# Kernel tuning notes

Measured on AMD Instinct MI355X. Metric: run time of the kernel, lower is better.

## Reference

```python
import jax, jax.numpy as jnp
import numpy as np

D_MODEL = 512
N_HEADS = 8
D_K = D_MODEL // N_HEADS  # 64
EPS = 1e-5


def setup_inputs() -> dict:
    key = jax.random.key(0)
    ks = jax.random.split(key, 16)
    s = 0.02
    B, T = 4, 2048
    return {
        "x": jax.random.normal(ks[0], (B, T, D_MODEL), dtype=jnp.float32),
        # per-head q/k/v projections stacked over heads: [H, d_model, d_k]
        "Wq": jax.random.normal(ks[1], (N_HEADS, D_MODEL, D_K), dtype=jnp.float32) * s,
        "bq": jnp.zeros((N_HEADS, D_K), dtype=jnp.float32),
        "Wk": jax.random.normal(ks[2], (N_HEADS, D_MODEL, D_K), dtype=jnp.float32) * s,
        "bk": jnp.zeros((N_HEADS, D_K), dtype=jnp.float32),
        "Wv": jax.random.normal(ks[3], (N_HEADS, D_MODEL, D_K), dtype=jnp.float32) * s,
        "bv": jnp.zeros((N_HEADS, D_K), dtype=jnp.float32),
        "Wp": jax.random.normal(ks[4], (D_MODEL, D_MODEL), dtype=jnp.float32) * s,
        "bp": jnp.zeros((D_MODEL,), dtype=jnp.float32),
        "W1": jax.random.normal(ks[5], (D_MODEL, 4 * D_MODEL), dtype=jnp.float32) * s,
        "b1": jnp.zeros((4 * D_MODEL,), dtype=jnp.float32),
        "W2": jax.random.normal(ks[6], (4 * D_MODEL, D_MODEL), dtype=jnp.float32) * s,
        "b2": jnp.zeros((D_MODEL,), dtype=jnp.float32),
        "g1": jnp.ones((D_MODEL,), dtype=jnp.float32),
        "be1": jnp.zeros((D_MODEL,), dtype=jnp.float32),
        "g2": jnp.ones((D_MODEL,), dtype=jnp.float32),
        "be2": jnp.zeros((D_MODEL,), dtype=jnp.float32),
    }


def _layer_norm(x, g, b):
    mu = jnp.mean(x, axis=-1, keepdims=True)
    var = jnp.var(x, axis=-1, keepdims=True)
    return (x - mu) * jax.lax.rsqrt(var + EPS) * g + b


def _block(x, Wq, bq, Wk, bk, Wv, bv, Wp, bp, W1, b1, W2, b2, g1, be1, g2, be2):
    B, T, _ = x.shape
    h = _layer_norm(x, g1, be1)
    # batched per-head projections: [B, H, T, d_k]
    q = jnp.einsum('btd,hdk->bhtk', h, Wq) + bq[:, None, :]
    k = jnp.einsum('btd,hdk->bhtk', h, Wk) + bk[:, None, :]
    v = jnp.einsum('btd,hdk->bhtk', h, Wv) + bv[:, None, :]
    scores = jnp.einsum('bhtk,bhsk->bhts', q, k)  # [B, H, T, T]
    causal = jnp.tril(jnp.ones((T, T), dtype=bool))
    # faithful to source: mask with -1e9 BEFORE dividing by sqrt(d_k)
    scores = jnp.where(causal, scores, jnp.float32(-1e9))
    attn = jax.nn.softmax(scores / jnp.float32(np.sqrt(D_K)), axis=-1)
    o = jnp.einsum('bhts,bhsk->bhtk', attn, v)  # [B, H, T, d_k]
    o = o.transpose(0, 2, 1, 3).reshape(B, T, D_MODEL)  # concat heads
    x = x + o @ Wp + bp
    h2 = _layer_norm(x, g2, be2)
    ff = jax.nn.relu(h2 @ W1 + b1) @ W2 + b2
    return x + ff


def reference(x, Wq, bq, Wk, bk, Wv, bv, Wp, bp, W1, b1, W2, b2, g1, be1, g2, be2):
    return _block(x, Wq, bq, Wk, bk, Wv, bv, Wp, bp, W1, b1, W2, b2, g1, be1, g2, be2)
```

## Files before the change

### kernel.cpp

```cpp
#include <hip/hip_runtime.h>
#include <hip/hip_bf16.h>
#include <math.h>

#define BATCH 4
#define SEQ   2048
#define DM    512
#define NH    8
#define DK    64
#define FF    2048
#define BT    (BATCH * SEQ)

#define SCALE_Q 0.18033688011112042f

typedef short bf16x8 __attribute__((ext_vector_type(8)));
typedef float f32x4  __attribute__((ext_vector_type(4)));

static __device__ inline short f2bf(float f) {
  union { float f; unsigned u; } v; v.f = f;
  unsigned r = (v.u + 0x7fffu + ((v.u >> 16) & 1u)) >> 16;
  return (short)r;
}

static __device__ __forceinline__ void gload16(const short* g, short* l) {
  __builtin_amdgcn_global_load_lds(
      (const __attribute__((address_space(1))) void*)g,
      (__attribute__((address_space(3))) void*)l, 16, 0, 0);
}

static __device__ __forceinline__ void xcd_swizzle(int& bx, int& by) {
  int gx = gridDim.x;
  int nwg = gx * gridDim.y;
  int id = blockIdx.x + gx * blockIdx.y;
  int nid = (id & 7) * (nwg >> 3) + (id >> 3);
  bx = nid % gx;
  by = nid / gx;
}

__global__ __launch_bounds__(256) void ln_kernel(
    const float* __restrict__ x, const float* __restrict__ gamma,
    const float* __restrict__ beta, short* __restrict__ out) {
  int row = blockIdx.x;
  const float* xr = x + (size_t)row * DM;
  int t = threadIdx.x;
  float v0 = xr[t], v1 = xr[t + 256];
  float s = v0 + v1;
  float sq = v0 * v0 + v1 * v1;
  for (int off = 32; off; off >>= 1) {
    s  += __shfl_xor(s, off);
    sq += __shfl_xor(sq, off);
  }
  __shared__ float ssum[4], ssq[4];
  int wave = t >> 6, lane = t & 63;
  if (lane == 0) { ssum[wave] = s; ssq[wave] = sq; }
  __syncthreads();
  if (t == 0) {
    float S = ssum[0] + ssum[1] + ssum[2] + ssum[3];
    float Q = ssq[0] + ssq[1] + ssq[2] + ssq[3];
    float mu = S * (1.0f / DM);
    float var = Q * (1.0f / DM) - mu * mu;
    ssum[0] = mu;
    ssq[0] = rsqrtf(var + 1e-5f);
  }
  __syncthreads();
  float mu = ssum[0], rstd = ssq[0];
  short* orow = out + (size_t)row * DM;
  orow[t]       = f2bf((v0 - mu) * rstd * gamma[t]       + beta[t]);
  orow[t + 256] = f2bf((v1 - mu) * rstd * gamma[t + 256] + beta[t + 256]);
}

__global__ __launch_bounds__(256) void wconv_kernel(
    const float* Wq, const float* Wk, const float* Wv,
    const float* Wp, const float* W1, const float* W2,
    short* wqkv, short* wpt, short* w1t, short* w2t) {
  int id = blockIdx.x;
  const float* src; short* dst; int R, C, tx, ty;
  if (id < 192) {
    int z = id >> 3;
    int m = z >> 3, hh = z & 7;
    const float* s0 = (m == 0) ? Wq : (m == 1) ? Wk : Wv;
    src = s0 + (size_t)hh * 512 * 64;
    dst = wqkv + ((size_t)(m * 512 + hh * 64)) * 512;
    R = 512; C = 64; tx = 0; ty = id & 7;
  } else if (id < 256) {
    int w = id - 192; src = Wp; dst = wpt; R = 512; C = 512;
    tx = w & 7; ty = w >> 3;
  } else if (id < 512) {
    int w = id - 256; src = W1; dst = w1t; R = 512; C = 2048;
    tx = w & 31; ty = w >> 5;
  } else {
    int w = id - 512; src = W2; dst = w2t; R = 2048; C = 512;
    tx = w & 7; ty = w >> 3;
  }
  __shared__ float Ts[64][68];
  int t = threadIdx.x;
  int r = t >> 2, c0 = (t & 3) * 16;
  const float* sp = src + (size_t)(ty * 64 + r) * C + tx * 64 + c0;
#pragma unroll
  for (int i = 0; i < 16; i += 4) {
    float4 v = *(const float4*)(sp + i);
    Ts[c0 + i + 0][r] = v.x; Ts[c0 + i + 1][r] = v.y;
    Ts[c0 + i + 2][r] = v.z; Ts[c0 + i + 3][r] = v.w;
  }
  __syncthreads();
  short* dp = dst + (size_t)(tx * 64 + r) * R + ty * 64 + c0;
  short tmp[16];
#pragma unroll
  for (int i = 0; i < 16; ++i) tmp[i] = f2bf(Ts[r][c0 + i]);
  *(int4*)(dp)     = *(int4*)&tmp[0];
  *(int4*)(dp + 8) = *(int4*)&tmp[8];
}

template<int TM, int TN>
__device__ __forceinline__ void gemm_core(
    const short* __restrict__ A, const short* __restrict__ Bw,
    int m0, int n0, int K, short* smem, f32x4 (&acc)[TM / 32][TN / 32]) {
  constexpr int AF = TM / 32, BF = TN / 32;
  constexpr int AC = TM / 64, BC = TN / 64;
  constexpr int BUFS = (TM + TN) * 32;
  int t = threadIdx.x;
  int wave = t >> 6, lane = t & 63, quad = lane >> 4, l16 = lane & 15;
  int wr = wave >> 1, wc = wave & 1;

  size_t aoff[AC], boff[BC];
  int aldsoff[AC], bldsoff[BC];
#pragma unroll
  for (int c = 0; c < AC; ++c) {
    int p = c * 256 + t, row = p >> 2, lg = (p & 3) ^ ((row >> 1) & 3);
    aoff[c] = (size_t)(m0 + row) * K + lg * 8;
    aldsoff[c] = c * 2048 + wave * 512;
  }
#pragma unroll
  for (int c = 0; c < BC; ++c) {
    int p = c * 256 + t, row = p >> 2, lg = (p & 3) ^ ((row >> 1) & 3);
    boff[c] = (size_t)(n0 + row) * K + lg * 8;
    bldsoff[c] = TM * 32 + c * 2048 + wave * 512;
  }

#pragma unroll
  for (int c = 0; c < AC; ++c) gload16(A + aoff[c], smem + aldsoff[c]);
#pragma unroll
  for (int c = 0; c < BC; ++c) gload16(Bw + boff[c], smem + bldsoff[c]);

  int physo = (quad ^ ((l16 >> 1) & 3)) * 8;

  for (int k0 = 0; k0 < K; k0 += 32) {
    short* cbuf = smem + ((k0 >> 5) & 1) * BUFS;
    __syncthreads();
    if (k0 + 32 < K) {
      short* nbuf = smem + (((k0 >> 5) & 1) ^ 1) * BUFS;
#pragma unroll
      for (int c = 0; c < AC; ++c) gload16(A + aoff[c] + k0 + 32, nbuf + aldsoff[c]);
#pragma unroll
      for (int c = 0; c < BC; ++c) gload16(Bw + boff[c] + k0 + 32, nbuf + bldsoff[c]);
    }
    bf16x8 af[AF], bfr[BF];
#pragma unroll
    for (int i = 0; i < AF; ++i)
      af[i] = *(const bf16x8*)&cbuf[(wr * (TM / 2) + i * 16 + l16) * 32 + physo];
#pragma unroll
    for (int j = 0; j < BF; ++j)
      bfr[j] = *(const bf16x8*)&cbuf[TM * 32 + (wc * (TN / 2) + j * 16 + l16) * 32 + physo];
#pragma unroll
    for (int i = 0; i < AF; ++i)
#pragma unroll
      for (int j = 0; j < BF; ++j)
        acc[i][j] = __builtin_amdgcn_mfma_f32_16x16x32_bf16(bfr[j], af[i], acc[i][j], 0, 0, 0);
  }
}

__global__ __launch_bounds__(256) void mgemm64_kernel(
    const short* __restrict__ A, const short* __restrict__ Bw,
    const float* __restrict__ bias, const float* __restrict__ res,
    void* __restrict__ C, int N, int K, int dorelu, int bf16out) {
  __shared__ __align__(16) short smem[2 * 8192];
  f32x4 acc[2][2];
  f32x4 zf = {0.f, 0.f, 0.f, 0.f};
#pragma unroll
  for (int i = 0; i < 2; ++i)
#pragma unroll
    for (int j = 0; j < 2; ++j) acc[i][j] = zf;
  int bx, by;
  xcd_swizzle(bx, by);
  int m0 = by * 64, n0 = bx * 64;

  int t = threadIdx.x;
  int wave = t >> 6, lane = t & 63, quad = lane >> 4, l16 = lane & 15;
  int wr = wave >> 1, wc = wave & 1;

  int rA0 = t >> 3,        lg0 = (t & 7) ^ (rA0 & 7);
  int rA1 = 32 + (t >> 3), lg1 = (t & 7) ^ (rA1 & 7);
  size_t aoff0 = (size_t)(m0 + rA0) * K + lg0 * 8;
  size_t aoff1 = (size_t)(m0 + rA1) * K + lg1 * 8;
  size_t boff0 = (size_t)(n0 + rA0) * K + lg0 * 8;
  size_t boff1 = (size_t)(n0 + rA1) * K + lg1 * 8;
  int lo0 = wave * 512, lo1 = 2048 + wave * 512;

  gload16(A + aoff0, smem + lo0);
  gload16(A + aoff1, smem + lo1);
  gload16(Bw + boff0, smem + 4096 + lo0);
  gload16(Bw + boff1, smem + 4096 + lo1);

  int sw = l16 & 7;

  for (int k0 = 0; k0 < K; k0 += 64) {
    short* cbuf = smem + ((k0 >> 6) & 1) * 8192;
    __syncthreads();
    if (k0 + 64 < K) {
      short* nbuf = smem + (((k0 >> 6) & 1) ^ 1) * 8192;
      gload16(A + aoff0 + k0 + 64, nbuf + lo0);
      gload16(A + aoff1 + k0 + 64, nbuf + lo1);
      gload16(Bw + boff0 + k0 + 64, nbuf + 4096 + lo0);
      gload16(Bw + boff1 + k0 + 64, nbuf + 4096 + lo1);
    }
    bf16x8 af0[2], af1[2], bf0[2], bf1[2];
#pragma unroll
    for (int i = 0; i < 2; ++i) {
      int r = wr * 32 + i * 16 + l16;
      af0[i] = *(const bf16x8*)&cbuf[r * 64 + ((quad ^ sw) * 8)];
      af1[i] = *(const bf16x8*)&cbuf[r * 64 + (((4 + quad) ^ sw) * 8)];
    }
#pragma unroll
    for (int j = 0; j < 2; ++j) {
      int r = wc * 32 + j * 16 + l16;
      bf0[j] = *(const bf16x8*)&cbuf[4096 + r * 64 + ((quad ^ sw) * 8)];
      bf1[j] = *(const bf16x8*)&cbuf[4096 + r * 64 + (((4 + quad) ^ sw) * 8)];
    }
#pragma unroll
    for (int i = 0; i < 2; ++i)
#pragma unroll
      for (int j = 0; j < 2; ++j) {
        acc[i][j] = __builtin_amdgcn_mfma_f32_16x16x32_bf16(bf0[j], af0[i], acc[i][j], 0, 0, 0);
        acc[i][j] = __builtin_amdgcn_mfma_f32_16x16x32_bf16(bf1[j], af1[i], acc[i][j], 0, 0, 0);
      }
  }

#pragma unroll
  for (int i = 0; i < 2; ++i) {
    int m = m0 + wr * 32 + i * 16 + l16;
#pragma unroll
    for (int j = 0; j < 2; ++j) {
      int nb = n0 + wc * 32 + j * 16 + quad * 4;
      float4 bv = *(const float4*)&bias[nb];
      float v[4] = {acc[i][j][0] + bv.x, acc[i][j][1] + bv.y,
                    acc[i][j][2] + bv.z, acc[i][j][3] + bv.w};
      if (dorelu) {
#pragma unroll
        for (int r = 0; r < 4; ++r) v[r] = fmaxf(v[r], 0.0f);
      }
      size_t off = (size_t)m * N + nb;
      if (res) {
        float4 rv = *(const float4*)(res + off);
        v[0] += rv.x; v[1] += rv.y; v[2] += rv.z; v[3] += rv.w;
      }
      if (bf16out) {
        short tmp[4] = {f2bf(v[0]), f2bf(v[1]), f2bf(v[2]), f2bf(v[3])};
        *(int2*)((short*)C + off) = *(int2*)tmp;
      } else {
        float4 outv = {v[0], v[1], v[2], v[3]};
        *(float4*)((float*)C + off) = outv;
      }
    }
  }
}

__global__ __launch_bounds__(256) void qkv_kernel(
    const short* __restrict__ A, const short* __restrict__ Bw,
    const float* __restrict__ bq, const float* __restrict__ bk,
    const float* __restrict__ bv,
    short* __restrict__ q, short* __restrict__ k, short* __restrict__ vt) {
  __shared__ __align__(16) short smem[12288];
  f32x4 acc[4][2];
  f32x4 zf = {0.f, 0.f, 0.f, 0.f};
#pragma unroll
  for (int i = 0; i < 4; ++i)
#pragma unroll
    for (int j = 0; j < 2; ++j) acc[i][j] = zf;
  int bx, by;
  xcd_swizzle(bx, by);
  int m0 = by * 128, n0 = bx * 64;
  gemm_core<128, 64>(A, Bw, m0, n0, DM, smem, acc);

  int t = threadIdx.x;
  int wave = t >> 6, lane = t & 63, quad = lane >> 4, l16 = lane & 15;
  int wr = wave >> 1, wc = wave & 1;

  if (n0 < 1024) {
    short* out = (n0 < 512) ? q : k;
    const float* bias = (n0 < 512) ? bq + n0 : bk + (n0 - 512);
    float scale = (n0 < 512) ? SCALE_Q : 1.0f;
    int ncol0 = (n0 < 512) ? n0 : n0 - 512;
#pragma unroll
    for (int i = 0; i < 4; ++i) {
      int m = m0 + wr * 64 + i * 16 + l16;
#pragma unroll
      for (int j = 0; j < 2; ++j) {
        int nb = wc * 32 + j * 16 + quad * 4;
        float4 bvv = *(const float4*)&bias[nb];
        short tmp[4];
        tmp[0] = f2bf((acc[i][j][0] + bvv.x) * scale);
        tmp[1] = f2bf((acc[i][j][1] + bvv.y) * scale);
        tmp[2] = f2bf((acc[i][j][2] + bvv.z) * scale);
        tmp[3] = f2bf((acc[i][j][3] + bvv.w) * scale);
        *(int2*)(out + (size_t)m * DM + ncol0 + nb) = *(int2*)tmp;
      }
    }
  } else {
    const float* bias = bv + (n0 - 1024);
    __syncthreads();
    short* Ts = smem;
#pragma unroll
    for (int i = 0; i < 4; ++i) {
      int ml = wr * 64 + i * 16 + l16;
#pragma unroll
      for (int j = 0; j < 2; ++j) {
        int nb = wc * 32 + j * 16 + quad * 4;
        float4 bvv = *(const float4*)&bias[nb];
        Ts[(nb + 0) * 136 + ml] = f2bf(acc[i][j][0] + bvv.x);
        Ts[(nb + 1) * 136 + ml] = f2bf(acc[i][j][1] + bvv.y);
        Ts[(nb + 2) * 136 + ml] = f2bf(acc[i][j][2] + bvv.z);
        Ts[(nb + 3) * 136 + ml] = f2bf(acc[i][j][3] + bvv.w);
      }
    }
    __syncthreads();
    int nl = t >> 2, seg = (t & 3) * 32;
    int gn = (n0 - 1024) + nl;
    int hh = gn >> 6, dk = gn & 63;
    int bidx = m0 >> 11, s0 = (m0 & 2047) + seg;
    short* dst = vt + ((size_t)((bidx * NH + hh) * DK + dk)) * SEQ + s0;
    const short* srcT = &Ts[nl * 136 + seg];
#pragma unroll
    for (int i2 = 0; i2 < 32; i2 += 8)
      *(int4*)(dst + i2) = *(const int4*)(srcT + i2);
  }
}

template<bool DIAG>
static __device__ __forceinline__ void attn_tile(
    const short* __restrict__ KsC, const short* __restrict__ VsC,
    short* __restrict__ Psw, const bf16x8& qf0, const bf16x8& qf1,
    f32x4 (&o_acc)[4], float& l_part, int quad, int l16,
    int keyb0, int qrow) {
  f32x4 zf = {0.f, 0.f, 0.f, 0.f};
  int sw = l16 & 7;

#pragma unroll
  for (int nt = 0; nt < 4; ++nt) {
    int krow = nt * 16 + l16;
    bf16x8 ka0 = *(const bf16x8*)&KsC[krow * 64 + ((quad ^ sw) * 8)];
    bf16x8 ka1 = *(const bf16x8*)&KsC[krow * 64 + (((4 + quad) ^ sw) * 8)];
    f32x4 s = __builtin_amdgcn_mfma_f32_16x16x32_bf16(ka0, qf0, zf, 0, 0, 0);
    s = __builtin_amdgcn_mfma_f32_16x16x32_bf16(ka1, qf1, s, 0, 0, 0);
    int keyb = keyb0 + nt * 16 + quad * 4;
    float pr[4];
#pragma unroll
    for (int r = 0; r < 4; ++r) {
      float e = exp2f(s[r]);
      pr[r] = (DIAG && (keyb + r > qrow)) ? 0.0f : e;
      l_part += pr[r];
    }
    unsigned pk0 = __builtin_amdgcn_perm(
        __float_as_uint(pr[1]), __float_as_uint(pr[0]), 0x07060302u);
    unsigned pk1 = __builtin_amdgcn_perm(
        __float_as_uint(pr[3]), __float_as_uint(pr[2]), 0x07060302u);
    int2 w = {(int)pk0, (int)pk1};
    *(int2*)&Psw[l16 * 64 + (((nt * 2 + (quad >> 1)) ^ sw) << 3) +
                 ((quad & 1) * 4)] = w;
  }

  bf16x8 apf0 = *(const bf16x8*)&Psw[l16 * 64 + ((quad ^ sw) * 8)];
  bf16x8 apf1 = *(const bf16x8*)&Psw[l16 * 64 + (((4 + quad) ^ sw) * 8)];
  __builtin_amdgcn_s_setprio(1);
#pragma unroll
  for (int nt2 = 0; nt2 < 4; ++nt2) {
    int vrow = nt2 * 16 + l16;
    bf16x8 vf0 = *(const bf16x8*)&VsC[vrow * 64 + ((quad ^ sw) * 8)];
    bf16x8 vf1 = *(const bf16x8*)&VsC[vrow * 64 + (((4 + quad) ^ sw) * 8)];
    o_acc[nt2] = __builtin_amdgcn_mfma_f32_16x16x32_bf16(vf0, apf0, o_acc[nt2], 0, 0, 0);
    o_acc[nt2] = __builtin_amdgcn_mfma_f32_16x16x32_bf16(vf1, apf1, o_acc[nt2], 0, 0, 0);
  }
  __builtin_amdgcn_s_setprio(0);
}

__global__ __launch_bounds__(256) void fattn_kernel(
    const short* __restrict__ Q, const short* __restrict__ Kg,
    const short* __restrict__ Vt, short* __restrict__ O,
    float* __restrict__ pscr) {
  int id = blockIdx.x;
  int c = id & 7, j = id >> 3;
  int sub = j & 3, w = j >> 2;
  int g = c * 4 + sub;
  int h = g & 7, b = g >> 3;
  int qt, kt0, ktN, p = 0;
  bool split;
  if (w < 16)      { qt = 31 - w;        p = 0; kt0 = 0;  ktN = 16;     split = true;  }
  else if (w < 32) { qt = 31 - (w - 16); p = 1; kt0 = 16; ktN = qt + 1; split = true;  }
  else             { qt = 15 - (w - 32);        kt0 = 0;  ktN = qt + 1; split = false; }
  bool hasdiag = !(split && p == 0);
  int q0 = qt * 64;
  int t = threadIdx.x, wave = t >> 6, lane = t & 63, quad = lane >> 4, l16 = lane & 15;

  __shared__ __align__(16) short Ks[2][64 * 64];
  __shared__ __align__(16) short Vs[2][64 * 64];
  __shared__ __align__(16) short Ps[4][16 * 64];

  f32x4 zf = {0.f, 0.f, 0.f, 0.f};
  const short* qp = Q + ((size_t)(b * SEQ + q0 + wave * 16 + l16)) * DM + h * DK;
  bf16x8 qf0 = *(const bf16x8*)(qp + quad * 8);
  bf16x8 qf1 = *(const bf16x8*)(qp + 32 + quad * 8);

  f32x4 o_acc[4];
  float l_part = 0.0f;
#pragma unroll
  for (int i = 0; i < 4; ++i) o_acc[i] = zf;

  const short* kb = Kg + ((size_t)(b * SEQ)) * DM + h * DK;
  const short* vb = Vt + ((size_t)((b * NH + h) * DK)) * SEQ;

  int row0 = t >> 3,         lg0 = (t & 7) ^ (row0 & 7);
  int row1 = (256 + t) >> 3, lg1 = ((256 + t) & 7) ^ (row1 & 7);
  const short* kp0 = kb + (size_t)row0 * DM + lg0 * 8 + (size_t)kt0 * 64 * DM;
  const short* kp1 = kb + (size_t)row1 * DM + lg1 * 8 + (size_t)kt0 * 64 * DM;
  const short* vp0 = vb + (size_t)row0 * SEQ + lg0 * 8 + kt0 * 64;
  const short* vp1 = vb + (size_t)row1 * SEQ + lg1 * 8 + kt0 * 64;
  int lo0 = wave * 512, lo1 = 2048 + wave * 512;

#define STAGE_KV(B) do {                                     \
    gload16(kp0, &Ks[B][lo0]); gload16(kp1, &Ks[B][lo1]);    \
    gload16(vp0, &Vs[B][lo0]); gload16(vp1, &Vs[B][lo1]);    \
    kp0 += 64 * DM; kp1 += 64 * DM; vp0 += 64; vp1 += 64; } while (0)

  STAGE_KV(0);

  int qrow = q0 + wave * 16 + l16;
  short* Psw = &Ps[wave][0];

  int buf = 0;
  for (int kt = kt0; kt < ktN - 1; ++kt) {
    __syncthreads();
    STAGE_KV(buf ^ 1);
    attn_tile<false>(&Ks[buf][0], &Vs[buf][0], Psw, qf0, qf1,
                     o_acc, l_part, quad, l16, 0, qrow);
    buf ^= 1;
  }
  __syncthreads();
  if (hasdiag)
    attn_tile<true>(&Ks[buf][0], &Vs[buf][0], Psw, qf0, qf1,
                    o_acc, l_part, quad, l16, (ktN - 1) * 64, qrow);
  else
    attn_tile<false>(&Ks[buf][0], &Vs[buf][0], Psw, qf0, qf1,
                     o_acc, l_part, quad, l16, 0, qrow);

  float lf = l_part;
  lf += __shfl_xor(lf, 16);
  lf += __shfl_xor(lf, 32);

  if (!split) {
    float inv = 1.0f / lf;
    short* orow = O + ((size_t)(b * SEQ) + qrow) * DM + h * DK;
#pragma unroll
    for (int nt2 = 0; nt2 < 4; ++nt2) {
      short tmp[4];
#pragma unroll
      for (int r = 0; r < 4; ++r) tmp[r] = f2bf(o_acc[nt2][r] * inv);
      *(int2*)(orow + nt2 * 16 + quad * 4) = *(int2*)tmp;
    }
  } else {
    int pblk = g * 16 + (qt - 16);
    int srow = pblk * 64 + wave * 16 + l16;
    float* po = pscr + (size_t)p * (32768 * 64);
    float* pl = pscr + (size_t)2 * (32768 * 64) + (size_t)p * 32768;
#pragma unroll
    for (int nt2 = 0; nt2 < 4; ++nt2)
      *(f32x4*)&po[(size_t)srow * 64 + nt2 * 16 + quad * 4] = o_acc[nt2];
    if (lane < 16) pl[pblk * 64 + wave * 16 + lane] = lf;
  }
#undef STAGE_KV
}

__global__ __launch_bounds__(256) void cmb_kernel(
    const float* __restrict__ pscr, short* __restrict__ O) {
  int gid = blockIdx.x * 256 + threadIdx.x;
  int srow = gid >> 6, dk = gid & 63;
  const float* po0 = pscr;
  const float* po1 = pscr + (size_t)32768 * 64;
  const float* pl0 = pscr + (size_t)2 * 32768 * 64;
  const float* pl1 = pl0 + 32768;
  float v = po0[gid] + po1[gid];
  float l = pl0[srow] + pl1[srow];
  int g = srow >> 10, rem = srow & 1023;
  int qt = 16 + (rem >> 6), row = rem & 63;
  int b = g >> 3, h = g & 7;
  int qrow = qt * 64 + row;
  O[((size_t)(b * SEQ + qrow)) * DM + h * DK + dk] = f2bf(v / l);
}

extern "C" void kernel_launch(void* const* d_in, const int* in_sizes, int n_in,
                              void* d_out, int out_size, void* d_ws, size_t ws_size,
                              hipStream_t stream) {
  const float* x   = (const float*)d_in[0];
  const float* Wq  = (const float*)d_in[1];
  const float* bq  = (const float*)d_in[2];
  const float* Wk  = (const float*)d_in[3];
  const float* bk  = (const float*)d_in[4];
  const float* Wv  = (const float*)d_in[5];
  const float* bv  = (const float*)d_in[6];
  const float* Wp  = (const float*)d_in[7];
  const float* bp  = (const float*)d_in[8];
  const float* W1  = (const float*)d_in[9];
  const float* b1  = (const float*)d_in[10];
  const float* W2  = (const float*)d_in[11];
  const float* b2  = (const float*)d_in[12];
  const float* g1  = (const float*)d_in[13];
  const float* be1 = (const float*)d_in[14];
  const float* g2  = (const float*)d_in[15];
  const float* be2 = (const float*)d_in[16];
  float* out = (float*)d_out;

  char* wsb = (char*)d_ws;
  const size_t SB = (size_t)BT * DM * 2;
  short* h    = (short*)(wsb);
  short* q    = (short*)(wsb + SB);
  short* k    = (short*)(wsb + 2 * SB);
  short* vt   = (short*)(wsb + 3 * SB);
  short* o    = (short*)(wsb + 4 * SB);
  float* x2   = (float*)(wsb + 5 * SB);
  short* h2   = (short*)(wsb + 5 * SB + (size_t)BT * DM * 4);
  short* ff   = (short*)(wsb + 6 * SB + (size_t)BT * DM * 4);
  float* pscr = (float*)ff;
  short* wqkv = (short*)(wsb + 6 * SB + (size_t)BT * DM * 4 + (size_t)BT * FF * 2);
  short* wpt  = wqkv + 1536 * 512;
  short* w1t  = wpt + 512 * 512;
  short* w2t  = w1t + 2048 * 512;

  dim3 blk(256);

  wconv_kernel<<<dim3(768), blk, 0, stream>>>(Wq, Wk, Wv, Wp, W1, W2,
                                              wqkv, wpt, w1t, w2t);
  ln_kernel<<<BT, blk, 0, stream>>>(x, g1, be1, h);

  qkv_kernel<<<dim3(24, 64), blk, 0, stream>>>(h, wqkv, bq, bk, bv, q, k, vt);

  fattn_kernel<<<dim3(1536), blk, 0, stream>>>(q, k, vt, o, pscr);
  cmb_kernel<<<dim3(8192), blk, 0, stream>>>(pscr, o);

  mgemm64_kernel<<<dim3(8, 128), blk, 0, stream>>>(o, wpt, bp, x, x2, DM, DM, 0, 0);
  ln_kernel<<<BT, blk, 0, stream>>>(x2, g2, be2, h2);
  mgemm64_kernel<<<dim3(32, 128), blk, 0, stream>>>(h2, w1t, b1, nullptr, ff, FF, DM, 1, 1);
  mgemm64_kernel<<<dim3(8, 128), blk, 0, stream>>>(ff, w2t, b2, x2, out, DM, FF, 0, 0);
}
```

Baseline: 251.4 us.

## Process two 16-row query groups per wave in flash attention to reuse K/V fragments

```diff
diff --git a/kernel.cpp b/kernel.cpp
--- a/kernel.cpp
+++ b/kernel.cpp
@@ -335,11 +335,11 @@
 }
 
 template<bool DIAG>
-static __device__ __forceinline__ void attn_tile(
+static __device__ __forceinline__ void attn_tile2(
     const short* __restrict__ KsC, const short* __restrict__ VsC,
-    short* __restrict__ Psw, const bf16x8& qf0, const bf16x8& qf1,
-    f32x4 (&o_acc)[4], float& l_part, int quad, int l16,
-    int keyb0, int qrow) {
+    short* __restrict__ Psw, const bf16x8 (&qf)[2][2],
+    f32x4 (&o_acc)[2][4], float (&lp)[2], int quad, int l16,
+    int keyb0, int qrow0, int qrow1) {
   f32x4 zf = {0.f, 0.f, 0.f, 0.f};
   int sw = l16 & 7;
 
@@ -348,35 +348,52 @@
     int krow = nt * 16 + l16;
     bf16x8 ka0 = *(const bf16x8*)&KsC[krow * 64 + ((quad ^ sw) * 8)];
     bf16x8 ka1 = *(const bf16x8*)&KsC[krow * 64 + (((4 + quad) ^ sw) * 8)];
-    f32x4 s = __builtin_amdgcn_mfma_f32_16x16x32_bf16(ka0, qf0, zf, 0, 0, 0);
-    s = __builtin_amdgcn_mfma_f32_16x16x32_bf16(ka1, qf1, s, 0, 0, 0);
-    int keyb = keyb0 + nt * 16 + quad * 4;
-    float pr[4];
+    f32x4 s0 = __builtin_amdgcn_mfma_f32_16x16x32_bf16(ka0, qf[0][0], zf, 0, 0, 0);
+    s0 = __builtin_amdgcn_mfma_f32_16x16x32_bf16(ka1, qf[0][1], s0, 0, 0, 0);
+    f32x4 s1 = __builtin_amdgcn_mfma_f32_16x16x32_bf16(ka0, qf[1][0], zf, 0, 0, 0);
+    s1 = __builtin_amdgcn_mfma_f32_16x16x32_bf16(ka1, qf[1][1], s1, 0, 0, 0);
+    int keyq = keyb0 + nt * 16 + quad * 4;
+    float p0[4], p1[4];
 #pragma unroll
     for (int r = 0; r < 4; ++r) {
-      float e = exp2f(s[r]);
-      pr[r] = (DIAG && (keyb + r > qrow)) ? 0.0f : e;
-      l_part += pr[r];
-    }
-    unsigned pk0 = __builtin_amdgcn_perm(
-        __float_as_uint(pr[1]), __float_as_uint(pr[0]), 0x07060302u);
-    unsigned pk1 = __builtin_amdgcn_perm(
-        __float_as_uint(pr[3]), __float_as_uint(pr[2]), 0x07060302u);
-    int2 w = {(int)pk0, (int)pk1};
-    *(int2*)&Psw[l16 * 64 + (((nt * 2 + (quad >> 1)) ^ sw) << 3) +
-                 ((quad & 1) * 4)] = w;
-  }
-
-  bf16x8 apf0 = *(const bf16x8*)&Psw[l16 * 64 + ((quad ^ sw) * 8)];
-  bf16x8 apf1 = *(const bf16x8*)&Psw[l16 * 64 + (((4 + quad) ^ sw) * 8)];
+      float e = exp2f(s0[r]);
+      p0[r] = (DIAG && (keyq + r > qrow0)) ? 0.0f : e;
+    }
+    lp[0] += (p0[0] + p0[1]) + (p0[2] + p0[3]);
+#pragma unroll
+    for (int r = 0; r < 4; ++r) {
+      float e = exp2f(s1[r]);
+      p1[r] = (DIAG && (keyq + r > qrow1)) ? 0.0f : e;
+    }
+    lp[1] += (p1[0] + p1[1]) + (p1[2] + p1[3]);
+    unsigned a0 = __builtin_amdgcn_perm(
+        __float_as_uint(p0[1]), __float_as_uint(p0[0]), 0x07060302u);
+    unsigned a1 = __builtin_amdgcn_perm(
+        __float_as_uint(p0[3]), __float_as_uint(p0[2]), 0x07060302u);
+    int2 w0 = {(int)a0, (int)a1};
+    *(int2*)&Psw[l16 * 72 + nt * 16 + quad * 4] = w0;
+    unsigned b0 = __builtin_amdgcn_perm(
+        __float_as_uint(p1[1]), __float_as_uint(p1[0]), 0x07060302u);
+    unsigned b1 = __builtin_amdgcn_perm(
+        __float_as_uint(p1[3]), __float_as_uint(p1[2]), 0x07060302u);
+    int2 w1 = {(int)b0, (int)b1};
+    *(int2*)&Psw[(16 + l16) * 72 + nt * 16 + quad * 4] = w1;
+  }
+
+  bf16x8 ap00 = *(const bf16x8*)&Psw[l16 * 72 + quad * 8];
+  bf16x8 ap01 = *(const bf16x8*)&Psw[l16 * 72 + 32 + quad * 8];
+  bf16x8 ap10 = *(const bf16x8*)&Psw[(16 + l16) * 72 + quad * 8];
+  bf16x8 ap11 = *(const bf16x8*)&Psw[(16 + l16) * 72 + 32 + quad * 8];
   __builtin_amdgcn_s_setprio(1);
 #pragma unroll
   for (int nt2 = 0; nt2 < 4; ++nt2) {
-    int vrow = nt2 * 16 + l16;
-    bf16x8 vf0 = *(const bf16x8*)&VsC[vrow * 64 + ((quad ^ sw) * 8)];
-    bf16x8 vf1 = *(const bf16x8*)&VsC[vrow * 64 + (((4 + quad) ^ sw) * 8)];
-    o_acc[nt2] = __builtin_amdgcn_mfma_f32_16x16x32_bf16(vf0, apf0, o_acc[nt2], 0, 0, 0);
-    o_acc[nt2] = __builtin_amdgcn_mfma_f32_16x16x32_bf16(vf1, apf1, o_acc[nt2], 0, 0, 0);
+    int vrow = nt2 * 16 + l16, swv = vrow & 7;
+    bf16x8 vf0 = *(const bf16x8*)&VsC[vrow * 64 + ((quad ^ swv) * 8)];
+    bf16x8 vf1 = *(const bf16x8*)&VsC[vrow * 64 + (((4 + quad) ^ swv) * 8)];
+    o_acc[0][nt2] = __builtin_amdgcn_mfma_f32_16x16x32_bf16(vf0, ap00, o_acc[0][nt2], 0, 0, 0);
+    o_acc[0][nt2] = __builtin_amdgcn_mfma_f32_16x16x32_bf16(vf1, ap01, o_acc[0][nt2], 0, 0, 0);
+    o_acc[1][nt2] = __builtin_amdgcn_mfma_f32_16x16x32_bf16(vf0, ap10, o_acc[1][nt2], 0, 0, 0);
+    o_acc[1][nt2] = __builtin_amdgcn_mfma_f32_16x16x32_bf16(vf1, ap11, o_acc[1][nt2], 0, 0, 0);
   }
   __builtin_amdgcn_s_setprio(0);
 }
@@ -387,31 +404,39 @@
     float* __restrict__ pscr) {
   int id = blockIdx.x;
   int c = id & 7, j = id >> 3;
-  int sub = j & 3, w = j >> 2;
-  int g = c * 4 + sub;
+  int g = c * 4 + (j & 3);
+  int w = j >> 2;
   int h = g & 7, b = g >> 3;
-  int qt, kt0, ktN, p = 0;
+  int s, kt0, ktN, p = 0;
   bool split;
-  if (w < 16)      { qt = 31 - w;        p = 0; kt0 = 0;  ktN = 16;     split = true;  }
-  else if (w < 32) { qt = 31 - (w - 16); p = 1; kt0 = 16; ktN = qt + 1; split = true;  }
-  else             { qt = 15 - (w - 32);        kt0 = 0;  ktN = qt + 1; split = false; }
+  if (w < 8)       { s = 15 - w;        p = 0; kt0 = 0;     ktN = s + 1;     split = true;  }
+  else if (w < 16) { s = 15 - (w - 8);  p = 1; kt0 = s + 1; ktN = 2 * s + 2; split = true;  }
+  else             { s = 7 - (w - 16);         kt0 = 0;     ktN = 2 * s + 2; split = false; }
   bool hasdiag = !(split && p == 0);
-  int q0 = qt * 64;
+  int q0 = s * 128;
   int t = threadIdx.x, wave = t >> 6, lane = t & 63, quad = lane >> 4, l16 = lane & 15;
 
   __shared__ __align__(16) short Ks[2][64 * 64];
   __shared__ __align__(16) short Vs[2][64 * 64];
-  __shared__ __align__(16) short Ps[4][16 * 64];
+  __shared__ __align__(16) short Ps[4][32 * 72];
 
   f32x4 zf = {0.f, 0.f, 0.f, 0.f};
-  const short* qp = Q + ((size_t)(b * SEQ + q0 + wave * 16 + l16)) * DM + h * DK;
-  bf16x8 qf0 = *(const bf16x8*)(qp + quad * 8);
-  bf16x8 qf1 = *(const bf16x8*)(qp + 32 + quad * 8);
-
-  f32x4 o_acc[4];
-  float l_part = 0.0f;
-#pragma unroll
-  for (int i = 0; i < 4; ++i) o_acc[i] = zf;
+  int qrow0 = q0 + wave * 32 + l16;
+  int qrow1 = qrow0 + 16;
+  const short* qp0 = Q + ((size_t)(b * SEQ + qrow0)) * DM + h * DK;
+  const short* qp1 = Q + ((size_t)(b * SEQ + qrow1)) * DM + h * DK;
+  bf16x8 qf[2][2];
+  qf[0][0] = *(const bf16x8*)(qp0 + quad * 8);
+  qf[0][1] = *(const bf16x8*)(qp0 + 32 + quad * 8);
+  qf[1][0] = *(const bf16x8*)(qp1 + quad * 8);
+  qf[1][1] = *(const bf16x8*)(qp1 + 32 + quad * 8);
+
+  f32x4 o_acc[2][4];
+  float lp[2] = {0.0f, 0.0f};
+#pragma unroll
+  for (int gi = 0; gi < 2; ++gi)
+#pragma unroll
+    for (int i = 0; i < 4; ++i) o_acc[gi][i] = zf;
 
   const short* kb = Kg + ((size_t)(b * SEQ)) * DM + h * DK;
   const short* vb = Vt + ((size_t)((b * NH + h) * DK)) * SEQ;
@@ -431,48 +456,47 @@
 
   STAGE_KV(0);
 
-  int qrow = q0 + wave * 16 + l16;
   short* Psw = &Ps[wave][0];
-
   int buf = 0;
-  for (int kt = kt0; kt < ktN - 1; ++kt) {
+  for (int kt = kt0; kt < ktN; ++kt) {
     __syncthreads();
-    STAGE_KV(buf ^ 1);
-    attn_tile<false>(&Ks[buf][0], &Vs[buf][0], Psw, qf0, qf1,
-                     o_acc, l_part, quad, l16, 0, qrow);
+    if (kt + 1 < ktN) STAGE_KV(buf ^ 1);
+    if (hasdiag && kt >= ktN - 2)
+      attn_tile2<true>(&Ks[buf][0], &Vs[buf][0], Psw, qf,
+                       o_acc, lp, quad, l16, kt * 64, qrow0, qrow1);
+    else
+      attn_tile2<false>(&Ks[buf][0], &Vs[buf][0], Psw, qf,
+                        o_acc, lp, quad, l16, 0, qrow0, qrow1);
     buf ^= 1;
   }
-  __syncthreads();
-  if (hasdiag)
-    attn_tile<true>(&Ks[buf][0], &Vs[buf][0], Psw, qf0, qf1,
-                    o_acc, l_part, quad, l16, (ktN - 1) * 64, qrow);
-  else
-    attn_tile<false>(&Ks[buf][0], &Vs[buf][0], Psw, qf0, qf1,
-                     o_acc, l_part, quad, l16, 0, qrow);
-
-  float lf = l_part;
-  lf += __shfl_xor(lf, 16);
-  lf += __shfl_xor(lf, 32);
-
-  if (!split) {
-    float inv = 1.0f / lf;
-    short* orow = O + ((size_t)(b * SEQ) + qrow) * DM + h * DK;
-#pragma unroll
-    for (int nt2 = 0; nt2 < 4; ++nt2) {
-      short tmp[4];
-#pragma unroll
-      for (int r = 0; r < 4; ++r) tmp[r] = f2bf(o_acc[nt2][r] * inv);
-      *(int2*)(orow + nt2 * 16 + quad * 4) = *(int2*)tmp;
-    }
-  } else {
-    int pblk = g * 16 + (qt - 16);
-    int srow = pblk * 64 + wave * 16 + l16;
-    float* po = pscr + (size_t)p * (32768 * 64);
-    float* pl = pscr + (size_t)2 * (32768 * 64) + (size_t)p * 32768;
-#pragma unroll
-    for (int nt2 = 0; nt2 < 4; ++nt2)
-      *(f32x4*)&po[(size_t)srow * 64 + nt2 * 16 + quad * 4] = o_acc[nt2];
-    if (lane < 16) pl[pblk * 64 + wave * 16 + lane] = lf;
+
+#pragma unroll
+  for (int gi = 0; gi < 2; ++gi) {
+    float lf = lp[gi];
+    lf += __shfl_xor(lf, 16);
+    lf += __shfl_xor(lf, 32);
+    int qrow = (gi == 0) ? qrow0 : qrow1;
+    if (!split) {
+      float inv = 1.0f / lf;
+      short* orow = O + ((size_t)(b * SEQ) + qrow) * DM + h * DK;
+#pragma unroll
+      for (int nt2 = 0; nt2 < 4; ++nt2) {
+        short tmp[4];
+#pragma unroll
+        for (int r = 0; r < 4; ++r) tmp[r] = f2bf(o_acc[gi][nt2][r] * inv);
+        *(int2*)(orow + nt2 * 16 + quad * 4) = *(int2*)tmp;
+      }
+    } else {
+      int pblk = g * 8 + (s - 8);
+      int lrow = wave * 32 + gi * 16 + l16;
+      int srow = pblk * 128 + lrow;
+      float* po = pscr + (size_t)p * (32768 * 64);
+      float* pl = pscr + (size_t)2 * (32768 * 64) + (size_t)p * 32768;
+#pragma unroll
+      for (int nt2 = 0; nt2 < 4; ++nt2)
+        *(f32x4*)&po[(size_t)srow * 64 + nt2 * 16 + quad * 4] = o_acc[gi][nt2];
+      if (lane < 16) pl[pblk * 128 + wave * 32 + gi * 16 + lane] = lf;
+    }
   }
 #undef STAGE_KV
 }
@@ -487,10 +511,10 @@
   const float* pl1 = pl0 + 32768;
   float v = po0[gid] + po1[gid];
   float l = pl0[srow] + pl1[srow];
-  int g = srow >> 10, rem = srow & 1023;
-  int qt = 16 + (rem >> 6), row = rem & 63;
+  int pblk = srow >> 7, r128 = srow & 127;
+  int g = pblk >> 3, s = 8 + (pblk & 7);
   int b = g >> 3, h = g & 7;
-  int qrow = qt * 64 + row;
+  int qrow = s * 128 + r128;
   O[((size_t)(b * SEQ + qrow)) * DM + h * DK + dk] = f2bf(v / l);
 }
 
@@ -540,7 +564,7 @@
 
   qkv_kernel<<<dim3(24, 64), blk, 0, stream>>>(h, wqkv, bq, bk, bv, q, k, vt);
 
-  fattn_kernel<<<dim3(1536), blk, 0, stream>>>(q, k, vt, o, pscr);
+  fattn_kernel<<<dim3(768), blk, 0, stream>>>(q, k, vt, o, pscr);
   cmb_kernel<<<dim3(8192), blk, 0, stream>>>(pscr, o);
 
   mgemm64_kernel<<<dim3(8, 128), blk, 0, stream>>>(o, wpt, bp, x, x2, DM, DM, 0, 0);
```

After: 270.1 us. 7.4% more time.

## Replace double-buffered LDS direct loads with register prefetch and single LDS buffer

Applied to the files above, without the earlier changes.

```diff
diff --git a/kernel.cpp b/kernel.cpp
--- a/kernel.cpp
+++ b/kernel.cpp
@@ -381,7 +381,7 @@
   __builtin_amdgcn_s_setprio(0);
 }
 
-__global__ __launch_bounds__(256) void fattn_kernel(
+__global__ __launch_bounds__(256, 6) void fattn_kernel(
     const short* __restrict__ Q, const short* __restrict__ Kg,
     const short* __restrict__ Vt, short* __restrict__ O,
     float* __restrict__ pscr) {
@@ -399,8 +399,8 @@
   int q0 = qt * 64;
   int t = threadIdx.x, wave = t >> 6, lane = t & 63, quad = lane >> 4, l16 = lane & 15;
 
-  __shared__ __align__(16) short Ks[2][64 * 64];
-  __shared__ __align__(16) short Vs[2][64 * 64];
+  __shared__ __align__(16) short Ks[64 * 64];
+  __shared__ __align__(16) short Vs[64 * 64];
   __shared__ __align__(16) short Ps[4][16 * 64];
 
   f32x4 zf = {0.f, 0.f, 0.f, 0.f};
@@ -422,33 +422,38 @@
   const short* kp1 = kb + (size_t)row1 * DM + lg1 * 8 + (size_t)kt0 * 64 * DM;
   const short* vp0 = vb + (size_t)row0 * SEQ + lg0 * 8 + kt0 * 64;
   const short* vp1 = vb + (size_t)row1 * SEQ + lg1 * 8 + kt0 * 64;
-  int lo0 = wave * 512, lo1 = 2048 + wave * 512;
-
-#define STAGE_KV(B) do {                                     \
-    gload16(kp0, &Ks[B][lo0]); gload16(kp1, &Ks[B][lo1]);    \
-    gload16(vp0, &Vs[B][lo0]); gload16(vp1, &Vs[B][lo1]);    \
+
+  int4 rk0, rk1, rv0, rv1;
+#define LOAD_KV() do {                                        \
+    rk0 = *(const int4*)kp0; rk1 = *(const int4*)kp1;         \
+    rv0 = *(const int4*)vp0; rv1 = *(const int4*)vp1;         \
     kp0 += 64 * DM; kp1 += 64 * DM; vp0 += 64; vp1 += 64; } while (0)
-
-  STAGE_KV(0);
+#define WRITE_KV() do {                                       \
+    *(int4*)&Ks[t * 8] = rk0; *(int4*)&Ks[2048 + t * 8] = rk1; \
+    *(int4*)&Vs[t * 8] = rv0; *(int4*)&Vs[2048 + t * 8] = rv1; } while (0)
+
+  LOAD_KV();
+  WRITE_KV();
+  __syncthreads();
 
   int qrow = q0 + wave * 16 + l16;
   short* Psw = &Ps[wave][0];
 
-  int buf = 0;
-  for (int kt = kt0; kt < ktN - 1; ++kt) {
-    __syncthreads();
-    STAGE_KV(buf ^ 1);
-    attn_tile<false>(&Ks[buf][0], &Vs[buf][0], Psw, qf0, qf1,
-                     o_acc, l_part, quad, l16, 0, qrow);
-    buf ^= 1;
-  }
-  __syncthreads();
-  if (hasdiag)
-    attn_tile<true>(&Ks[buf][0], &Vs[buf][0], Psw, qf0, qf1,
-                    o_acc, l_part, quad, l16, (ktN - 1) * 64, qrow);
-  else
-    attn_tile<false>(&Ks[buf][0], &Vs[buf][0], Psw, qf0, qf1,
-                     o_acc, l_part, quad, l16, 0, qrow);
+  for (int kt = kt0; kt < ktN; ++kt) {
+    bool more = (kt + 1 < ktN);
+    if (more) LOAD_KV();
+    if (hasdiag && kt == ktN - 1)
+      attn_tile<true>(Ks, Vs, Psw, qf0, qf1,
+                      o_acc, l_part, quad, l16, kt * 64, qrow);
+    else
+      attn_tile<false>(Ks, Vs, Psw, qf0, qf1,
+                       o_acc, l_part, quad, l16, 0, qrow);
+    if (more) {
+      __syncthreads();
+      WRITE_KV();
+      __syncthreads();
+    }
+  }
 
   float lf = l_part;
   lf += __shfl_xor(lf, 16);
@@ -475,6 +480,8 @@
     if (lane < 16) pl[pblk * 64 + wave * 16 + lane] = lf;
   }
 #undef STAGE_KV
+#undef LOAD_KV
+#undef WRITE_KV
 }
 
 __global__ __launch_bounds__(256) void cmb_kernel(
```

After: 292.5 us. 1.16x slower.
